# Performance work log

Hardware: AMD Instinct MI355X
Metric: run time of the kernel (lower is better)

The kernel has to match this reference:

```python
import jax, jax.numpy as jnp
import numpy as np

DMODEL = 512
NUM_HEADS = 8
HEAD_DIM = DMODEL // NUM_HEADS


def setup_inputs() -> dict:
    key = jax.random.key(0)
    k1, k2, k3, k4, k5 = jax.random.split(key, 5)
    x = jax.random.normal(k1, (4, 2048, DMODEL), dtype=jnp.float32)
    s = 1.0 / np.sqrt(DMODEL)
    W_qkv = jax.random.uniform(k2, (DMODEL, 3 * DMODEL), jnp.float32, -s, s)
    b_qkv = jax.random.uniform(k3, (3 * DMODEL,), jnp.float32, -s, s)
    W_out = jax.random.uniform(k4, (DMODEL, DMODEL), jnp.float32, -s, s)
    b_out = jax.random.uniform(k5, (DMODEL,), jnp.float32, -s, s)
    return {"x": x, "W_qkv": W_qkv, "b_qkv": b_qkv, "W_out": W_out, "b_out": b_out}


def reference(x, W_qkv, b_qkv, W_out, b_out):
    B, T, D = x.shape
    H, Hd = NUM_HEADS, HEAD_DIM
    qkv = x @ W_qkv + b_qkv                      # [B, T, 3D]
    qkv = qkv.reshape(B, T, 3, H, Hd).transpose(2, 0, 3, 1, 4)  # [3, B, H, T, Hd]
    q, k, v = qkv[0], qkv[1], qkv[2]
    scores = jnp.einsum('bhqd,bhkd->bhqk', q, k) / np.sqrt(Hd)  # [B, H, T, T]
    causal = jnp.tril(jnp.ones((T, T), dtype=bool))
    scores = jnp.where(causal, scores, -jnp.inf)
    weights = jax.nn.softmax(scores, axis=-1)
    out = jnp.einsum('bhqk,bhkd->bhqd', weights, v)  # [B, H, T, Hd]
    out = out.transpose(0, 2, 1, 3).reshape(B, T, D)
    return out @ W_out + b_out
```

## Files before the change

### kernel.cpp

```cpp
#include <hip/hip_runtime.h>
#include <cstdint>
#include <cstddef>

#define D_MODEL 512
#define SEQ_T 2048
#define NHEADS 8
#define HDIM 64

typedef __attribute__((ext_vector_type(8))) short bf16x8;
typedef __attribute__((ext_vector_type(4))) float f32x4;
typedef __attribute__((ext_vector_type(16))) float f32x16;

__device__ __forceinline__ unsigned short f2bf(float f) {
  unsigned int u = __float_as_uint(f);
  u += 0x7FFFu + ((u >> 16) & 1u);
  return (unsigned short)(u >> 16);
}

__device__ __forceinline__ unsigned int pack_bf16(float lo, float hi) {
  unsigned int a = __float_as_uint(lo) + 0x8000u;
  unsigned int b = __float_as_uint(hi) + 0x8000u;
  return __builtin_amdgcn_perm(b, a, 0x07060302u);
}

#define QSCALE 0.18033688011112043f
#define SSHIFT 16.0f

__device__ __forceinline__ void async_lds16(const unsigned short* g,
                                            unsigned short* l) {
  __builtin_amdgcn_global_load_lds(
      (const __attribute__((address_space(1))) void*)g,
      (__attribute__((address_space(3))) void*)l, 16, 0, 0);
}

__global__ __launch_bounds__(256) void prep_kernel(
    const float* __restrict__ x, const float* __restrict__ W_qkv,
    const float* __restrict__ W_out, unsigned short* __restrict__ xb,
    unsigned short* __restrict__ Wqkt, unsigned short* __restrict__ Wot) {
  __shared__ float tile[64][65];
  const int bid = blockIdx.x;
  if (bid < 2048) {
    int i = (bid * 256 + threadIdx.x) * 8;
    float4 a = *(const float4*)(x + i);
    float4 b = *(const float4*)(x + i + 4);
    ushort4 lo = {f2bf(a.x), f2bf(a.y), f2bf(a.z), f2bf(a.w)};
    ushort4 hi = {f2bf(b.x), f2bf(b.y), f2bf(b.z), f2bf(b.w)};
    *(ushort4*)(xb + i) = lo;
    *(ushort4*)(xb + i + 4) = hi;
    return;
  }
  const float* src;
  unsigned short* dst;
  int R = 512, C, c0, r0;
  if (bid < 2048 + 192) {
    int t = bid - 2048;
    C = 1536; c0 = (t % 24) * 64; r0 = (t / 24) * 64;
    src = W_qkv; dst = Wqkt;
  } else {
    int t = bid - 2240;
    C = 512; c0 = (t & 7) * 64; r0 = (t >> 3) * 64;
    src = W_out; dst = Wot;
  }
  for (int i = threadIdx.x; i < 64 * 64; i += 256) {
    int r = i >> 6, c = i & 63;
    tile[r][c] = src[(size_t)(r0 + r) * C + c0 + c];
  }
  __syncthreads();
  for (int i = threadIdx.x; i < 64 * 64; i += 256) {
    int c = i >> 6, r = i & 63;
    dst[(size_t)(c0 + c) * R + r0 + r] = f2bf(tile[r][c]);
  }
}

__global__ __launch_bounds__(256) void gemm_qkv_mfma(
    const unsigned short* __restrict__ xb, const unsigned short* __restrict__ Wt,
    const float* __restrict__ bias, unsigned short* __restrict__ Qtb,
    unsigned short* __restrict__ Kb, unsigned short* __restrict__ Vtb) {
  __shared__ unsigned short As[128 * 64];
  __shared__ unsigned short Bs[128 * 64];
  const int tid = threadIdx.x;
  const int w = tid >> 6, lane = tid & 63;
  const int quad = lane >> 4, l15 = lane & 15;
  const int wm = w >> 1, wn = w & 1;
  const int m0 = blockIdx.x * 128, n0 = blockIdx.y * 128;

  const int srow = tid >> 3;
  const int schunk = (tid & 7) ^ (srow & 7);
  const unsigned short* ga = xb + (size_t)(m0 + srow) * 512 + schunk * 8;
  const unsigned short* gb = Wt + (size_t)(n0 + srow) * 512 + schunk * 8;
  unsigned short* lA = As + tid * 8;
  unsigned short* lB = Bs + tid * 8;

  f32x4 acc[4][4] = {};
  for (int k0 = 0; k0 < 512; k0 += 64) {
#pragma unroll
    for (int rr = 0; rr < 4; ++rr) {
      async_lds16(ga + (size_t)rr * 32 * 512 + k0, lA + rr * 2048);
      async_lds16(gb + (size_t)rr * 32 * 512 + k0, lB + rr * 2048);
    }
    __syncthreads();
    bf16x8 af[4][2], bfr[4][2];
#pragma unroll
    for (int mb = 0; mb < 4; ++mb) {
      int row = wm * 64 + mb * 16 + l15;
#pragma unroll
      for (int kk = 0; kk < 2; ++kk) {
        int slot = (kk * 4 + quad) ^ (row & 7);
        af[mb][kk] = *(const bf16x8*)&As[row * 64 + slot * 8];
      }
    }
#pragma unroll
    for (int nb = 0; nb < 4; ++nb) {
      int row = wn * 64 + nb * 16 + l15;
#pragma unroll
      for (int kk = 0; kk < 2; ++kk) {
        int slot = (kk * 4 + quad) ^ (row & 7);
        bfr[nb][kk] = *(const bf16x8*)&Bs[row * 64 + slot * 8];
      }
    }
#pragma unroll
    for (int mb = 0; mb < 4; ++mb)
#pragma unroll
      for (int nb = 0; nb < 4; ++nb) {
        acc[mb][nb] = __builtin_amdgcn_mfma_f32_16x16x32_bf16(
            af[mb][0], bfr[nb][0], acc[mb][nb], 0, 0, 0);
        acc[mb][nb] = __builtin_amdgcn_mfma_f32_16x16x32_bf16(
            af[mb][1], bfr[nb][1], acc[mb][nb], 0, 0, 0);
      }
    __syncthreads();
  }

  const int cbase = n0 + wn * 64;
  const int three = cbase >> 9;
  const int h = (cbase >> 6) & 7;
  const int bh = ((m0 >> 11) << 3) + h;
  const int t0 = (m0 & 2047) + wm * 64;
  float bv[4];
#pragma unroll
  for (int nb = 0; nb < 4; ++nb) bv[nb] = bias[cbase + nb * 16 + l15];

  if (three == 0) {
#pragma unroll
    for (int mb = 0; mb < 4; ++mb)
#pragma unroll
      for (int nb = 0; nb < 4; ++nb) {
        int trow = t0 + mb * 16 + quad * 4;
        ushort4 v = {f2bf((acc[mb][nb][0] + bv[nb]) * QSCALE),
                     f2bf((acc[mb][nb][1] + bv[nb]) * QSCALE),
                     f2bf((acc[mb][nb][2] + bv[nb]) * QSCALE),
                     f2bf((acc[mb][nb][3] + bv[nb]) * QSCALE)};
        *(ushort4*)(Qtb + ((size_t)bh * HDIM + nb * 16 + l15) * SEQ_T + trow) = v;
      }
  } else if (three == 2) {
#pragma unroll
    for (int mb = 0; mb < 4; ++mb)
#pragma unroll
      for (int nb = 0; nb < 4; ++nb) {
        int trow = t0 + mb * 16 + quad * 4;
        ushort4 v = {f2bf(acc[mb][nb][0] + bv[nb]), f2bf(acc[mb][nb][1] + bv[nb]),
                     f2bf(acc[mb][nb][2] + bv[nb]), f2bf(acc[mb][nb][3] + bv[nb])};
        *(ushort4*)(Vtb + ((size_t)bh * HDIM + nb * 16 + l15) * SEQ_T + trow) = v;
      }
  } else {
#pragma unroll
    for (int mb = 0; mb < 4; ++mb)
#pragma unroll
      for (int nb = 0; nb < 4; ++nb)
#pragma unroll
        for (int r = 0; r < 4; ++r) {
          int trow = t0 + mb * 16 + quad * 4 + r;
          Kb[((size_t)bh * SEQ_T + trow) * HDIM + nb * 16 + l15] =
              f2bf(acc[mb][nb][r] + bv[nb]);
        }
  }
}

__global__ __launch_bounds__(256, 2) void attn_mfma6(
    const unsigned short* __restrict__ Qtb, const unsigned short* __restrict__ Kb,
    const unsigned short* __restrict__ Vtb, unsigned short* __restrict__ AOb) {
  __shared__ __align__(16) unsigned short Ks[2][64 * 64];
  __shared__ __align__(16) unsigned short Vs[2][64 * 64];
  __shared__ __align__(16) unsigned short Pt[4][32 * 64];
  const int tid = threadIdx.x;
  const int w = tid >> 6, lane = tid & 63;
  const int l31 = lane & 31, h = lane >> 5;
  const int r7l = lane & 7;

  const int bid = blockIdx.x;
  const int xcd = bid & 7;
  const int j = bid >> 3;
  const int c = j & 31, g = j >> 5;
  const int kslot = c >> 2;
  const int bh = xcd + 8 * (c & 3);
  const int qt2 = g ? kslot : (15 - kslot);
  const int nmain = 2 * qt2;

  const unsigned short* kbase = Kb + (size_t)bh * SEQ_T * HDIM;
  const unsigned short* vbase = Vtb + (size_t)bh * HDIM * SEQ_T;
  const int sr = tid >> 3;
  const int lc = tid & 7;
  const int scol = lc * 8;
  const int swc = (lc ^ (sr & 7)) * 8;

  const int qglob = qt2 * 128 + w * 32 + l31;
  bf16x8 qf[4];
  {
    unsigned short qraw[32];
    const unsigned short* qp =
        Qtb + ((size_t)bh * HDIM + h * 8) * SEQ_T + qglob;
#pragma unroll
    for (int cc = 0; cc < 4; ++cc)
#pragma unroll
      for (int jj = 0; jj < 8; ++jj)
        qraw[cc * 8 + jj] = qp[(size_t)(cc * 16 + jj) * SEQ_T];
#pragma unroll
    for (int cc = 0; cc < 4; ++cc) qf[cc] = *(const bf16x8*)(qraw + cc * 8);
  }

  f32x16 O0 = {0.f, 0.f, 0.f, 0.f, 0.f, 0.f, 0.f, 0.f,
               0.f, 0.f, 0.f, 0.f, 0.f, 0.f, 0.f, 0.f};
  f32x16 O1 = O0;
  float l_acc = 0.f;

  auto tile_compute = [&](int cur, int lim, bool masked) {
    f32x16 S0 = {0.f, 0.f, 0.f, 0.f, 0.f, 0.f, 0.f, 0.f,
                 0.f, 0.f, 0.f, 0.f, 0.f, 0.f, 0.f, 0.f};
    f32x16 S1 = S0;
#pragma unroll
    for (int cc = 0; cc < 4; ++cc) {
      const int slot = ((cc << 1) | h) ^ r7l;
      const bf16x8 k0 = *(const bf16x8*)&Ks[cur][l31 * 64 + slot * 8];
      const bf16x8 k1 = *(const bf16x8*)&Ks[cur][(32 + l31) * 64 + slot * 8];
      S0 = __builtin_amdgcn_mfma_f32_32x32x16_bf16(k0, qf[cc], S0, 0, 0, 0);
      S1 = __builtin_amdgcn_mfma_f32_32x32x16_bf16(k1, qf[cc], S1, 0, 0, 0);
    }
#pragma unroll
    for (int m = 0; m < 8; ++m) {
      float p0 = __builtin_amdgcn_exp2f(S0[2 * m] - SSHIFT);
      float p1 = __builtin_amdgcn_exp2f(S0[2 * m + 1] - SSHIFT);
      float p2 = __builtin_amdgcn_exp2f(S1[2 * m] - SSHIFT);
      float p3 = __builtin_amdgcn_exp2f(S1[2 * m + 1] - SSHIFT);
      if (masked) {
        const int r0 = 2 * m, r1 = 2 * m + 1;
        const int kl0 = (r0 & 3) + 8 * (r0 >> 2) + 4 * h;
        const int kl1 = (r1 & 3) + 8 * (r1 >> 2) + 4 * h;
        p0 = (kl0 > lim) ? 0.f : p0;
        p1 = (kl1 > lim) ? 0.f : p1;
        p2 = (kl0 + 32 > lim) ? 0.f : p2;
        p3 = (kl1 + 32 > lim) ? 0.f : p3;
      }
      l_acc += (p0 + p1) + (p2 + p3);
      const int within = 2 * (m & 1) + 4 * h;
      const int slot0 = (m >> 1) ^ r7l;
      const int slot1 = ((m >> 1) + 4) ^ r7l;
      *(unsigned int*)&Pt[w][l31 * 64 + slot0 * 8 + within] = pack_bf16(p0, p1);
      *(unsigned int*)&Pt[w][l31 * 64 + slot1 * 8 + within] = pack_bf16(p2, p3);
    }
#pragma unroll
    for (int t = 0; t < 4; ++t) {
      const int slot = ((t << 1) | h) ^ r7l;
      const bf16x8 pb = *(const bf16x8*)&Pt[w][l31 * 64 + slot * 8];
      const bf16x8 v0 = *(const bf16x8*)&Vs[cur][l31 * 64 + slot * 8];
      const bf16x8 v1 = *(const bf16x8*)&Vs[cur][(32 + l31) * 64 + slot * 8];
      O0 = __builtin_amdgcn_mfma_f32_32x32x16_bf16(v0, pb, O0, 0, 0, 0);
      O1 = __builtin_amdgcn_mfma_f32_32x32x16_bf16(v1, pb, O1, 0, 0, 0);
    }
  };

  {
    const unsigned short* kp = kbase + (size_t)sr * 64 + scol;
    uint4 rk0 = *(const uint4*)kp;
    uint4 rk1 = *(const uint4*)(kp + 32 * 64);
    const unsigned short* vp = vbase + (size_t)sr * SEQ_T + scol;
    uint4 rv0 = *(const uint4*)vp;
    uint4 rv1 = *(const uint4*)(vp + 32 * SEQ_T);
    *(uint4*)&Ks[0][sr * 64 + swc] = rk0;
    *(uint4*)&Ks[0][(sr + 32) * 64 + swc] = rk1;
    *(uint4*)&Vs[0][sr * 64 + swc] = rv0;
    *(uint4*)&Vs[0][(sr + 32) * 64 + swc] = rv1;
  }
  __syncthreads();

  for (int i = 0; i < nmain; ++i) {
    const int cur = i & 1;
    uint4 rk0, rk1, rv0, rv1;
    {
      const int nkt = i + 1;
      const unsigned short* kp = kbase + (size_t)(nkt * 64 + sr) * 64 + scol;
      rk0 = *(const uint4*)kp;
      rk1 = *(const uint4*)(kp + 32 * 64);
      const unsigned short* vp = vbase + (size_t)sr * SEQ_T + nkt * 64 + scol;
      rv0 = *(const uint4*)vp;
      rv1 = *(const uint4*)(vp + 32 * SEQ_T);
    }
    tile_compute(cur, 0, false);
    const int nxt = cur ^ 1;
    *(uint4*)&Ks[nxt][sr * 64 + swc] = rk0;
    *(uint4*)&Ks[nxt][(sr + 32) * 64 + swc] = rk1;
    *(uint4*)&Vs[nxt][sr * 64 + swc] = rv0;
    *(uint4*)&Vs[nxt][(sr + 32) * 64 + swc] = rv1;
    __syncthreads();
  }

  {
    const int cur = nmain & 1;
    const int nkt = nmain + 1;
    const unsigned short* kp = kbase + (size_t)(nkt * 64 + sr) * 64 + scol;
    uint4 rk0 = *(const uint4*)kp;
    uint4 rk1 = *(const uint4*)(kp + 32 * 64);
    const unsigned short* vp = vbase + (size_t)sr * SEQ_T + nkt * 64 + scol;
    uint4 rv0 = *(const uint4*)vp;
    uint4 rv1 = *(const uint4*)(vp + 32 * SEQ_T);
    tile_compute(cur, w * 32 + l31, true);
    const int nxt = cur ^ 1;
    *(uint4*)&Ks[nxt][sr * 64 + swc] = rk0;
    *(uint4*)&Ks[nxt][(sr + 32) * 64 + swc] = rk1;
    *(uint4*)&Vs[nxt][sr * 64 + swc] = rv0;
    *(uint4*)&Vs[nxt][(sr + 32) * 64 + swc] = rv1;
    __syncthreads();
  }

  if (w >= 2) {
    const int cur = (nmain + 1) & 1;
    tile_compute(cur, w * 32 + l31 - 64, true);
  }

  l_acc += __shfl_xor(l_acc, 32, 64);
  const float inv = 1.0f / fmaxf(l_acc, 1e-30f);
  const int bb = bh >> 3, hh = bh & 7;
  unsigned short* dst = AOb + ((size_t)bb * SEQ_T + qglob) * D_MODEL + (hh << 6);
#pragma unroll
  for (int rg = 0; rg < 4; ++rg) {
    ushort4 o0 = {f2bf(O0[4 * rg + 0] * inv), f2bf(O0[4 * rg + 1] * inv),
                  f2bf(O0[4 * rg + 2] * inv), f2bf(O0[4 * rg + 3] * inv)};
    *(ushort4*)(dst + 8 * rg + 4 * h) = o0;
    ushort4 o1 = {f2bf(O1[4 * rg + 0] * inv), f2bf(O1[4 * rg + 1] * inv),
                  f2bf(O1[4 * rg + 2] * inv), f2bf(O1[4 * rg + 3] * inv)};
    *(ushort4*)(dst + 32 + 8 * rg + 4 * h) = o1;
  }
}

__global__ __launch_bounds__(256) void gemm_out_mfma(
    const unsigned short* __restrict__ AOb, const unsigned short* __restrict__ Wot,
    const float* __restrict__ bias, float* __restrict__ out) {
  __shared__ unsigned short As[64 * 64];
  __shared__ unsigned short Bs[128 * 64];
  const int tid = threadIdx.x;
  const int w = tid >> 6, lane = tid & 63;
  const int quad = lane >> 4, l15 = lane & 15;
  const int m0 = blockIdx.x * 64, n0 = blockIdx.y * 128;

  const int srow = tid >> 3;
  const int schunk = (tid & 7) ^ (srow & 7);
  const unsigned short* ga = AOb + (size_t)(m0 + srow) * 512 + schunk * 8;
  const unsigned short* gb = Wot + (size_t)(n0 + srow) * 512 + schunk * 8;
  unsigned short* lA = As + tid * 8;
  unsigned short* lB = Bs + tid * 8;

  f32x4 acc[4][2] = {};
  for (int k0 = 0; k0 < 512; k0 += 64) {
#pragma unroll
    for (int rr = 0; rr < 2; ++rr)
      async_lds16(ga + (size_t)rr * 32 * 512 + k0, lA + rr * 2048);
#pragma unroll
    for (int rr = 0; rr < 4; ++rr)
      async_lds16(gb + (size_t)rr * 32 * 512 + k0, lB + rr * 2048);
    __syncthreads();
    bf16x8 af[4][2], bfr[2][2];
#pragma unroll
    for (int mb = 0; mb < 4; ++mb) {
      int row = mb * 16 + l15;
#pragma unroll
      for (int kk = 0; kk < 2; ++kk) {
        int slot = (kk * 4 + quad) ^ (row & 7);
        af[mb][kk] = *(const bf16x8*)&As[row * 64 + slot * 8];
      }
    }
#pragma unroll
    for (int nb = 0; nb < 2; ++nb) {
      int row = w * 32 + nb * 16 + l15;
#pragma unroll
      for (int kk = 0; kk < 2; ++kk) {
        int slot = (kk * 4 + quad) ^ (row & 7);
        bfr[nb][kk] = *(const bf16x8*)&Bs[row * 64 + slot * 8];
      }
    }
#pragma unroll
    for (int mb = 0; mb < 4; ++mb)
#pragma unroll
      for (int nb = 0; nb < 2; ++nb) {
        acc[mb][nb] = __builtin_amdgcn_mfma_f32_16x16x32_bf16(
            af[mb][0], bfr[nb][0], acc[mb][nb], 0, 0, 0);
        acc[mb][nb] = __builtin_amdgcn_mfma_f32_16x16x32_bf16(
            af[mb][1], bfr[nb][1], acc[mb][nb], 0, 0, 0);
      }
    __syncthreads();
  }

  const int cbase = n0 + w * 32;
  float bv[2];
#pragma unroll
  for (int nb = 0; nb < 2; ++nb) bv[nb] = bias[cbase + nb * 16 + l15];
#pragma unroll
  for (int mb = 0; mb < 4; ++mb)
#pragma unroll
    for (int nb = 0; nb < 2; ++nb)
#pragma unroll
      for (int r = 0; r < 4; ++r)
        out[(size_t)(m0 + mb * 16 + quad * 4 + r) * 512 + cbase + nb * 16 +
            l15] = acc[mb][nb][r] + bv[nb];
}

extern "C" void kernel_launch(void* const* d_in, const int* in_sizes, int n_in,
                              void* d_out, int out_size, void* d_ws,
                              size_t ws_size, hipStream_t stream) {
  const float* x     = (const float*)d_in[0];
  const float* W_qkv = (const float*)d_in[1];
  const float* b_qkv = (const float*)d_in[2];
  const float* W_out = (const float*)d_in[3];
  const float* b_out = (const float*)d_in[4];
  float* out = (float*)d_out;

  const size_t NX = (size_t)4 * SEQ_T * D_MODEL;
  unsigned short* xb   = (unsigned short*)d_ws;
  unsigned short* Wqkt = xb + NX;
  unsigned short* Wot  = Wqkt + (size_t)1536 * 512;
  unsigned short* Qtb  = Wot + (size_t)512 * 512;
  unsigned short* Kb   = Qtb + NX;
  unsigned short* Vtb  = Kb + NX;
  unsigned short* AOb  = Vtb + NX;

  prep_kernel<<<2304, 256, 0, stream>>>(x, W_qkv, W_out, xb, Wqkt, Wot);
  gemm_qkv_mfma<<<dim3(64, 12), 256, 0, stream>>>(xb, Wqkt, b_qkv, Qtb, Kb,
                                                  Vtb);
  attn_mfma6<<<dim3(512), 256, 0, stream>>>(Qtb, Kb, Vtb, AOb);
  gemm_out_mfma<<<dim3(128, 4), 256, 0, stream>>>(AOb, Wot, b_out, out);
}
```

Measured before the change: 147.8 us.

## Keep P in registers via permlane swap and stage K/V with async LDS loads

The attention kernel no longer writes P to a per-wave LDS buffer and reads it back. It packs P to bf16 in registers and rearranges halves across lanes with permlane32_swap, producing the B operand for the PV MFMA directly. K/V tile staging now uses direct global-to-LDS async loads with swizzled source addresses instead of register round trips. MFMA sections are wrapped in s_setprio. This drops LDS traffic and register pressure, but relies on the async load completing before the barrier and on the permlane layout matching the MFMA operand layout.

```diff
diff --git a/kernel.cpp b/kernel.cpp
--- a/kernel.cpp
+++ b/kernel.cpp
@@ -10,6 +10,7 @@
 typedef __attribute__((ext_vector_type(8))) short bf16x8;
 typedef __attribute__((ext_vector_type(4))) float f32x4;
 typedef __attribute__((ext_vector_type(16))) float f32x16;
+typedef __attribute__((ext_vector_type(2))) unsigned int uint2v;
 
 __device__ __forceinline__ unsigned short f2bf(float f) {
   unsigned int u = __float_as_uint(f);
@@ -21,6 +22,12 @@
   unsigned int a = __float_as_uint(lo) + 0x8000u;
   unsigned int b = __float_as_uint(hi) + 0x8000u;
   return __builtin_amdgcn_perm(b, a, 0x07060302u);
+}
+
+__device__ __forceinline__ void plswap(unsigned int& a, unsigned int& b) {
+  uint2v r = __builtin_amdgcn_permlane32_swap(a, b, false, false);
+  a = r[0];
+  b = r[1];
 }
 
 #define QSCALE 0.18033688011112043f
@@ -175,12 +182,11 @@
   }
 }
 
-__global__ __launch_bounds__(256, 2) void attn_mfma6(
+__global__ __launch_bounds__(256, 2) void attn_mfma7(
     const unsigned short* __restrict__ Qtb, const unsigned short* __restrict__ Kb,
     const unsigned short* __restrict__ Vtb, unsigned short* __restrict__ AOb) {
   __shared__ __align__(16) unsigned short Ks[2][64 * 64];
   __shared__ __align__(16) unsigned short Vs[2][64 * 64];
-  __shared__ __align__(16) unsigned short Pt[4][32 * 64];
   const int tid = threadIdx.x;
   const int w = tid >> 6, lane = tid & 63;
   const int l31 = lane & 31, h = lane >> 5;
@@ -199,8 +205,16 @@
   const unsigned short* vbase = Vtb + (size_t)bh * HDIM * SEQ_T;
   const int sr = tid >> 3;
   const int lc = tid & 7;
-  const int scol = lc * 8;
-  const int swc = (lc ^ (sr & 7)) * 8;
+  const int sw8 = (lc ^ (sr & 7)) * 8;
+
+  auto stage = [&](int b, int kt) {
+    const unsigned short* kp = kbase + (size_t)(kt * 64 + sr) * 64 + sw8;
+    async_lds16(kp, &Ks[b][tid * 8]);
+    async_lds16(kp + 32 * 64, &Ks[b][2048 + tid * 8]);
+    const unsigned short* vp = vbase + (size_t)sr * SEQ_T + kt * 64 + sw8;
+    async_lds16(vp, &Vs[b][tid * 8]);
+    async_lds16(vp + (size_t)32 * SEQ_T, &Vs[b][2048 + tid * 8]);
+  };
 
   const int qglob = qt2 * 128 + w * 32 + l31;
   bf16x8 qf[4];
@@ -226,6 +240,7 @@
     f32x16 S0 = {0.f, 0.f, 0.f, 0.f, 0.f, 0.f, 0.f, 0.f,
                  0.f, 0.f, 0.f, 0.f, 0.f, 0.f, 0.f, 0.f};
     f32x16 S1 = S0;
+    __builtin_amdgcn_s_setprio(1);
 #pragma unroll
     for (int cc = 0; cc < 4; ++cc) {
       const int slot = ((cc << 1) | h) ^ r7l;
@@ -234,6 +249,8 @@
       S0 = __builtin_amdgcn_mfma_f32_32x32x16_bf16(k0, qf[cc], S0, 0, 0, 0);
       S1 = __builtin_amdgcn_mfma_f32_32x32x16_bf16(k1, qf[cc], S1, 0, 0, 0);
     }
+    __builtin_amdgcn_s_setprio(0);
+    unsigned int pk0[8], pk1[8];
 #pragma unroll
     for (int m = 0; m < 8; ++m) {
       float p0 = __builtin_amdgcn_exp2f(S0[2 * m] - SSHIFT);
@@ -250,73 +267,53 @@
         p3 = (kl1 + 32 > lim) ? 0.f : p3;
       }
       l_acc += (p0 + p1) + (p2 + p3);
-      const int within = 2 * (m & 1) + 4 * h;
-      const int slot0 = (m >> 1) ^ r7l;
-      const int slot1 = ((m >> 1) + 4) ^ r7l;
-      *(unsigned int*)&Pt[w][l31 * 64 + slot0 * 8 + within] = pack_bf16(p0, p1);
-      *(unsigned int*)&Pt[w][l31 * 64 + slot1 * 8 + within] = pack_bf16(p2, p3);
-    }
-#pragma unroll
-    for (int t = 0; t < 4; ++t) {
-      const int slot = ((t << 1) | h) ^ r7l;
-      const bf16x8 pb = *(const bf16x8*)&Pt[w][l31 * 64 + slot * 8];
-      const bf16x8 v0 = *(const bf16x8*)&Vs[cur][l31 * 64 + slot * 8];
-      const bf16x8 v1 = *(const bf16x8*)&Vs[cur][(32 + l31) * 64 + slot * 8];
-      O0 = __builtin_amdgcn_mfma_f32_32x32x16_bf16(v0, pb, O0, 0, 0, 0);
-      O1 = __builtin_amdgcn_mfma_f32_32x32x16_bf16(v1, pb, O1, 0, 0, 0);
-    }
+      pk0[m] = pack_bf16(p0, p1);
+      pk1[m] = pack_bf16(p2, p3);
+    }
+#pragma unroll
+    for (int tp = 0; tp < 2; ++tp) {
+      plswap(pk0[4 * tp + 0], pk0[4 * tp + 2]);
+      plswap(pk0[4 * tp + 1], pk0[4 * tp + 3]);
+      plswap(pk1[4 * tp + 0], pk1[4 * tp + 2]);
+      plswap(pk1[4 * tp + 1], pk1[4 * tp + 3]);
+    }
+#pragma unroll
+    for (int kb = 0; kb < 2; ++kb)
+#pragma unroll
+      for (int tp = 0; tp < 2; ++tp) {
+        const int t = 2 * kb + tp;
+        uint4 wv;
+        if (kb == 0)
+          wv = (uint4){pk0[4 * tp + 0], pk0[4 * tp + 1], pk0[4 * tp + 2],
+                       pk0[4 * tp + 3]};
+        else
+          wv = (uint4){pk1[4 * tp + 0], pk1[4 * tp + 1], pk1[4 * tp + 2],
+                       pk1[4 * tp + 3]};
+        const bf16x8 pb = *(const bf16x8*)&wv;
+        const int slot = ((t << 1) | h) ^ r7l;
+        const bf16x8 v0 = *(const bf16x8*)&Vs[cur][l31 * 64 + slot * 8];
+        const bf16x8 v1 = *(const bf16x8*)&Vs[cur][(32 + l31) * 64 + slot * 8];
+        __builtin_amdgcn_s_setprio(1);
+        O0 = __builtin_amdgcn_mfma_f32_32x32x16_bf16(v0, pb, O0, 0, 0, 0);
+        O1 = __builtin_amdgcn_mfma_f32_32x32x16_bf16(v1, pb, O1, 0, 0, 0);
+        __builtin_amdgcn_s_setprio(0);
+      }
   };
 
-  {
-    const unsigned short* kp = kbase + (size_t)sr * 64 + scol;
-    uint4 rk0 = *(const uint4*)kp;
-    uint4 rk1 = *(const uint4*)(kp + 32 * 64);
-    const unsigned short* vp = vbase + (size_t)sr * SEQ_T + scol;
-    uint4 rv0 = *(const uint4*)vp;
-    uint4 rv1 = *(const uint4*)(vp + 32 * SEQ_T);
-    *(uint4*)&Ks[0][sr * 64 + swc] = rk0;
-    *(uint4*)&Ks[0][(sr + 32) * 64 + swc] = rk1;
-    *(uint4*)&Vs[0][sr * 64 + swc] = rv0;
-    *(uint4*)&Vs[0][(sr + 32) * 64 + swc] = rv1;
-  }
+  stage(0, 0);
   __syncthreads();
 
   for (int i = 0; i < nmain; ++i) {
     const int cur = i & 1;
-    uint4 rk0, rk1, rv0, rv1;
-    {
-      const int nkt = i + 1;
-      const unsigned short* kp = kbase + (size_t)(nkt * 64 + sr) * 64 + scol;
-      rk0 = *(const uint4*)kp;
-      rk1 = *(const uint4*)(kp + 32 * 64);
-      const unsigned short* vp = vbase + (size_t)sr * SEQ_T + nkt * 64 + scol;
-      rv0 = *(const uint4*)vp;
-      rv1 = *(const uint4*)(vp + 32 * SEQ_T);
-    }
+    stage(cur ^ 1, i + 1);
     tile_compute(cur, 0, false);
-    const int nxt = cur ^ 1;
-    *(uint4*)&Ks[nxt][sr * 64 + swc] = rk0;
-    *(uint4*)&Ks[nxt][(sr + 32) * 64 + swc] = rk1;
-    *(uint4*)&Vs[nxt][sr * 64 + swc] = rv0;
-    *(uint4*)&Vs[nxt][(sr + 32) * 64 + swc] = rv1;
     __syncthreads();
   }
 
   {
     const int cur = nmain & 1;
-    const int nkt = nmain + 1;
-    const unsigned short* kp = kbase + (size_t)(nkt * 64 + sr) * 64 + scol;
-    uint4 rk0 = *(const uint4*)kp;
-    uint4 rk1 = *(const uint4*)(kp + 32 * 64);
-    const unsigned short* vp = vbase + (size_t)sr * SEQ_T + nkt * 64 + scol;
-    uint4 rv0 = *(const uint4*)vp;
-    uint4 rv1 = *(const uint4*)(vp + 32 * SEQ_T);
+    stage(cur ^ 1, nmain + 1);
     tile_compute(cur, w * 32 + l31, true);
-    const int nxt = cur ^ 1;
-    *(uint4*)&Ks[nxt][sr * 64 + swc] = rk0;
-    *(uint4*)&Ks[nxt][(sr + 32) * 64 + swc] = rk1;
-    *(uint4*)&Vs[nxt][sr * 64 + swc] = rv0;
-    *(uint4*)&Vs[nxt][(sr + 32) * 64 + swc] = rv1;
     __syncthreads();
   }
 
@@ -433,6 +430,6 @@
   prep_kernel<<<2304, 256, 0, stream>>>(x, W_qkv, W_out, xb, Wqkt, Wot);
   gemm_qkv_mfma<<<dim3(64, 12), 256, 0, stream>>>(xb, Wqkt, b_qkv, Qtb, Kb,
                                                   Vtb);
-  attn_mfma6<<<dim3(512), 256, 0, stream>>>(Qtb, Kb, Vtb, AOb);
+  attn_mfma7<<<dim3(512), 256, 0, stream>>>(Qtb, Kb, Vtb, AOb);
   gemm_out_mfma<<<dim3(128, 4), 256, 0, stream>>>(AOb, Wot, b_out, out);
 }
```

New measurement: 147.3 us. About the same (-0.3%).
